# Optimization experiments

Hardware: AMD Instinct MI355X
Metric: run time of the kernel (lower is better)

The kernel has to match this reference:

```python
import jax, jax.numpy as jnp
import numpy as np

D = 2048
N_HEAD = 16
D_HEAD = D // N_HEAD
EXP = 4
EPS = 1e-6


def setup_inputs() -> dict:
    key = jax.random.key(0)
    ks = jax.random.split(key, 8)
    b, s = 2, 2048
    scale = 0.02
    return {
        "x": jax.random.normal(ks[0], (b, s, D), dtype=jnp.float32),
        "w_qkv": jax.random.normal(ks[1], (D, 3 * D), dtype=jnp.float32) * scale,
        "w_o": jax.random.normal(ks[2], (D, D), dtype=jnp.float32) * scale,
        "w_up": jax.random.normal(ks[3], (D, EXP * D), dtype=jnp.float32) * scale,
        "w_gate": jax.random.normal(ks[4], (D, EXP * D), dtype=jnp.float32) * scale,
        "w_down": jax.random.normal(ks[5], (EXP * D, D), dtype=jnp.float32) * scale,
        "scale1": jnp.ones((D,), dtype=jnp.float32),
        "scale2": jnp.ones((D,), dtype=jnp.float32),
    }


def _rmsnorm(x, scale):
    rms = jnp.sqrt(jnp.mean(x * x, axis=-1, keepdims=True) + EPS)
    return x / rms * scale


def _attention(x, w_qkv, w_o):
    b, s, d = x.shape
    qkv = x @ w_qkv  # [b, s, 3d]
    q, k, v = jnp.split(qkv, 3, axis=-1)
    # [b, h, s, dh]
    q = q.reshape(b, s, N_HEAD, D_HEAD).transpose(0, 2, 1, 3)
    k = k.reshape(b, s, N_HEAD, D_HEAD).transpose(0, 2, 1, 3)
    v = v.reshape(b, s, N_HEAD, D_HEAD).transpose(0, 2, 1, 3)
    scores = jnp.einsum("bhqd,bhkd->bhqk", q, k) / np.sqrt(D_HEAD).astype(np.float32)
    causal = jnp.tril(jnp.ones((s, s), dtype=bool))
    scores = jnp.where(causal, scores, -jnp.inf)
    attn = jax.nn.softmax(scores, axis=-1)
    out = jnp.einsum("bhqk,bhkd->bhqd", attn, v)
    out = out.transpose(0, 2, 1, 3).reshape(b, s, d)
    return out @ w_o


def _mlp(x, w_up, w_gate, w_down):
    return (x @ w_up * jax.nn.silu(x @ w_gate)) @ w_down


def reference(x, w_qkv, w_o, w_up, w_gate, w_down, scale1, scale2):
    x = x + _attention(_rmsnorm(x, scale1), w_qkv, w_o)
    x = x + _mlp(_rmsnorm(x, scale2), w_up, w_gate, w_down)
    return x
```

## Files before the change

kernel.cpp:

```cpp
#include <hip/hip_runtime.h>

typedef unsigned short u16;
typedef __bf16 bfrag8 __attribute__((ext_vector_type(8)));
typedef float f32x4 __attribute__((ext_vector_type(4)));

#define MFMA16(a, b, c) __builtin_amdgcn_mfma_f32_16x16x32_bf16((a), (b), (c), 0, 0, 0)

static __device__ __forceinline__ u16 bf_bits(float f) {
  unsigned int u = __builtin_bit_cast(unsigned int, f);
  unsigned int r = (u + 0x7fffu + ((u >> 16) & 1u)) >> 16;
  return (u16)r;
}
static __device__ __forceinline__ float f_from_bits(u16 u) {
  unsigned int w = ((unsigned int)u) << 16;
  return __builtin_bit_cast(float, w);
}
static __device__ __forceinline__ void gload16(const void* g, void* l) {
  __builtin_amdgcn_global_load_lds(
      (const __attribute__((address_space(1))) void*)g,
      (__attribute__((address_space(3))) void*)l, 16, 0, 0);
}

__global__ __launch_bounds__(256) void k_transpose_bf16(const float* __restrict__ src,
                                                        u16* __restrict__ dst,
                                                        int K, int N) {
  __shared__ float tile[32][33];
  const int n0 = blockIdx.x * 32;
  const int k0 = blockIdx.y * 32;
  const int t = threadIdx.x;
  const int lr = t >> 5;
  const int lc = t & 31;
#pragma unroll
  for (int i = 0; i < 4; ++i)
    tile[lr + i * 8][lc] = src[(size_t)(k0 + lr + i * 8) * N + n0 + lc];
  __syncthreads();
#pragma unroll
  for (int i = 0; i < 4; ++i)
    dst[(size_t)(n0 + lr + i * 8) * K + k0 + lc] = bf_bits(tile[lc][lr + i * 8]);
}

__global__ __launch_bounds__(256) void k_transpose_v(const u16* __restrict__ qkv,
                                                     u16* __restrict__ vtg) {
  __shared__ u16 tile[32][33];
  const int bh = blockIdx.z, b = bh >> 4, hh = bh & 15;
  const int s0 = blockIdx.x * 32, d0 = blockIdx.y * 32;
  const int t = threadIdx.x;
  const int lr = t >> 5, lc = t & 31;
#pragma unroll
  for (int i = 0; i < 4; ++i)
    tile[lr + i * 8][lc] =
        qkv[(size_t)(b * 2048 + s0 + lr + i * 8) * 6144 + 4096 + hh * 128 + d0 + lc];
  __syncthreads();
#pragma unroll
  for (int i = 0; i < 4; ++i)
    vtg[(size_t)bh * 128 * 2048 + (size_t)(d0 + lr + i * 8) * 2048 + s0 + lc] =
        tile[lc][lr + i * 8];
}

__global__ __launch_bounds__(256) void k_rmsnorm(const float* __restrict__ x,
                                                 const float* __restrict__ sc,
                                                 u16* __restrict__ o) {
  const int row = blockIdx.x;
  const int t = threadIdx.x;
  const float4* x4 = (const float4*)(x + (size_t)row * 2048);
  float4 a = x4[t];
  float4 b = x4[t + 256];
  float ss = a.x * a.x + a.y * a.y + a.z * a.z + a.w * a.w +
             b.x * b.x + b.y * b.y + b.z * b.z + b.w * b.w;
#pragma unroll
  for (int off = 32; off > 0; off >>= 1) ss += __shfl_down(ss, off);
  __shared__ float red[4];
  if ((t & 63) == 0) red[t >> 6] = ss;
  __syncthreads();
  const float inv = rsqrtf((red[0] + red[1] + red[2] + red[3]) * (1.0f / 2048.0f) + 1e-6f);
  const float4* s4 = (const float4*)sc;
  float4 sa = s4[t], sb = s4[t + 256];
  ushort4 pa, pb;
  pa.x = bf_bits(a.x * inv * sa.x); pa.y = bf_bits(a.y * inv * sa.y);
  pa.z = bf_bits(a.z * inv * sa.z); pa.w = bf_bits(a.w * inv * sa.w);
  pb.x = bf_bits(b.x * inv * sb.x); pb.y = bf_bits(b.y * inv * sb.y);
  pb.z = bf_bits(b.z * inv * sb.z); pb.w = bf_bits(b.w * inv * sb.w);
  *(ushort4*)(o + (size_t)row * 2048 + t * 4) = pa;
  *(ushort4*)(o + (size_t)row * 2048 + (t + 256) * 4) = pb;
}

template <int EPI, int K, int PART>
__global__ __launch_bounds__(256, 3) void k_gemm2(const u16* __restrict__ A,
                                                  const u16* __restrict__ Bt,
                                                  int N,
                                                  float* __restrict__ outF,
                                                  u16* __restrict__ outB,
                                                  const float* __restrict__ resid) {
  __shared__ u16 sm[24576];
  char* smC = (char*)sm;
  const int nbx = gridDim.x;
  const int f = blockIdx.x + nbx * blockIdx.y;
  int m0, np;
  if (PART == 0) {
    const int nsl = nbx >> 3;
    const int x = f & 7;
    const int j = f >> 3;
    np = x * nsl + (j % nsl);
    m0 = (j / nsl) * 128;
  } else {
    const int msl = (int)gridDim.y >> 3;
    const int x = f & 7;
    const int j = f >> 3;
    m0 = (x * msl + (j % msl)) * 128;
    np = j / msl;
  }
  const int n0 = np * 256;

  const int t = threadIdx.x;
  const int wid = t >> 6, lane = t & 63;
  const int wm = wid >> 1, wn = wid & 1;
  const int l15 = lane & 15, lhi = lane >> 4;
  const int lhi16 = lhi * 16;
  const int swz = (l15 & 7) << 4;

  f32x4 acc0[4][4], acc1[4][4];
#pragma unroll
  for (int i = 0; i < 4; ++i)
#pragma unroll
    for (int j2 = 0; j2 < 4; ++j2) {
      acc0[i][j2] = (f32x4){0.f, 0.f, 0.f, 0.f};
      acc1[i][j2] = (f32x4){0.f, 0.f, 0.f, 0.f};
    }

  const int sr = lane >> 3;
  const int csw = (((lane & 7) * 16) ^ (sr << 4)) >> 1;
  const u16* Asrc = A + (size_t)(m0 + wid * 32 + sr) * K + csw;
  const u16* B0src = Bt + (size_t)(n0 + wid * 32 + sr) * K + csw;
  const u16* B1src = Bt + (size_t)(n0 + 128 + wid * 32 + sr) * K + csw;
  char* adst = smC + wid * 4096 + lane * 16;
  char* b0dst = smC + 16384 + wid * 4096 + lane * 16;
  char* b1dst = smC + 32768 + wid * 4096 + lane * 16;

  for (int kt = 0; kt < K / 64; ++kt) {
    __syncthreads();
    const u16* as = Asrc + kt * 64;
    const u16* b0s = B0src + kt * 64;
    const u16* b1s = B1src + kt * 64;
#pragma unroll
    for (int c = 0; c < 4; ++c) {
      gload16(as + (size_t)c * 8 * K, adst + c * 1024);
      gload16(b0s + (size_t)c * 8 * K, b0dst + c * 1024);
      gload16(b1s + (size_t)c * 8 * K, b1dst + c * 1024);
    }
    asm volatile("s_waitcnt vmcnt(0)" ::: "memory");
    __syncthreads();

#pragma unroll
    for (int kh = 0; kh < 2; ++kh) {
      const int ko = (kh * 64 + lhi16);
      bfrag8 a0 = *(const bfrag8*)(smC + (wm * 64 + 0 * 16 + l15) * 128 + (ko ^ swz));
      bfrag8 a1 = *(const bfrag8*)(smC + (wm * 64 + 1 * 16 + l15) * 128 + (ko ^ swz));
      bfrag8 a2 = *(const bfrag8*)(smC + (wm * 64 + 2 * 16 + l15) * 128 + (ko ^ swz));
      bfrag8 a3 = *(const bfrag8*)(smC + (wm * 64 + 3 * 16 + l15) * 128 + (ko ^ swz));
      bfrag8 g0 = *(const bfrag8*)(smC + 16384 + (wn * 64 + 0 * 16 + l15) * 128 + (ko ^ swz));
      bfrag8 g1 = *(const bfrag8*)(smC + 16384 + (wn * 64 + 1 * 16 + l15) * 128 + (ko ^ swz));
      bfrag8 g2 = *(const bfrag8*)(smC + 16384 + (wn * 64 + 2 * 16 + l15) * 128 + (ko ^ swz));
      bfrag8 g3 = *(const bfrag8*)(smC + 16384 + (wn * 64 + 3 * 16 + l15) * 128 + (ko ^ swz));
      acc0[0][0] = MFMA16(a0, g0, acc0[0][0]); acc0[0][1] = MFMA16(a0, g1, acc0[0][1]);
      acc0[0][2] = MFMA16(a0, g2, acc0[0][2]); acc0[0][3] = MFMA16(a0, g3, acc0[0][3]);
      acc0[1][0] = MFMA16(a1, g0, acc0[1][0]); acc0[1][1] = MFMA16(a1, g1, acc0[1][1]);
      acc0[1][2] = MFMA16(a1, g2, acc0[1][2]); acc0[1][3] = MFMA16(a1, g3, acc0[1][3]);
      acc0[2][0] = MFMA16(a2, g0, acc0[2][0]); acc0[2][1] = MFMA16(a2, g1, acc0[2][1]);
      acc0[2][2] = MFMA16(a2, g2, acc0[2][2]); acc0[2][3] = MFMA16(a2, g3, acc0[2][3]);
      acc0[3][0] = MFMA16(a3, g0, acc0[3][0]); acc0[3][1] = MFMA16(a3, g1, acc0[3][1]);
      acc0[3][2] = MFMA16(a3, g2, acc0[3][2]); acc0[3][3] = MFMA16(a3, g3, acc0[3][3]);
      bfrag8 u0 = *(const bfrag8*)(smC + 32768 + (wn * 64 + 0 * 16 + l15) * 128 + (ko ^ swz));
      bfrag8 u1 = *(const bfrag8*)(smC + 32768 + (wn * 64 + 1 * 16 + l15) * 128 + (ko ^ swz));
      bfrag8 u2 = *(const bfrag8*)(smC + 32768 + (wn * 64 + 2 * 16 + l15) * 128 + (ko ^ swz));
      bfrag8 u3 = *(const bfrag8*)(smC + 32768 + (wn * 64 + 3 * 16 + l15) * 128 + (ko ^ swz));
      acc1[0][0] = MFMA16(a0, u0, acc1[0][0]); acc1[0][1] = MFMA16(a0, u1, acc1[0][1]);
      acc1[0][2] = MFMA16(a0, u2, acc1[0][2]); acc1[0][3] = MFMA16(a0, u3, acc1[0][3]);
      acc1[1][0] = MFMA16(a1, u0, acc1[1][0]); acc1[1][1] = MFMA16(a1, u1, acc1[1][1]);
      acc1[1][2] = MFMA16(a1, u2, acc1[1][2]); acc1[1][3] = MFMA16(a1, u3, acc1[1][3]);
      acc1[2][0] = MFMA16(a2, u0, acc1[2][0]); acc1[2][1] = MFMA16(a2, u1, acc1[2][1]);
      acc1[2][2] = MFMA16(a2, u2, acc1[2][2]); acc1[2][3] = MFMA16(a2, u3, acc1[2][3]);
      acc1[3][0] = MFMA16(a3, u0, acc1[3][0]); acc1[3][1] = MFMA16(a3, u1, acc1[3][1]);
      acc1[3][2] = MFMA16(a3, u2, acc1[3][2]); acc1[3][3] = MFMA16(a3, u3, acc1[3][3]);
    }
  }

#pragma unroll
  for (int h = 0; h < 2; ++h) {
#pragma unroll
    for (int i = 0; i < 4; ++i) {
#pragma unroll
      for (int j2 = 0; j2 < 4; ++j2) {
        const int mr = m0 + wm * 64 + i * 16 + lhi * 4;
        const int nc = n0 + h * 128 + wn * 64 + j2 * 16 + l15;
#pragma unroll
        for (int r = 0; r < 4; ++r) {
          const size_t idx = (size_t)(mr + r) * N + nc;
          const float v = h ? acc1[i][j2][r] : acc0[i][j2][r];
          if (EPI == 0) {
            outB[idx] = bf_bits(v);
          } else {
            outF[idx] = resid[idx] + v;
          }
        }
      }
    }
  }
}

template <int K>
__global__ __launch_bounds__(256, 3) void k_gemm_mlp(const u16* __restrict__ A,
                                                     const u16* __restrict__ Bg,
                                                     const u16* __restrict__ Bu,
                                                     int N,
                                                     u16* __restrict__ outB) {
  __shared__ u16 sm[24576];
  char* smC = (char*)sm;
  const int nbx = gridDim.x;
  const int f = blockIdx.x + nbx * blockIdx.y;
  const int nsl = nbx >> 3;
  const int x = f & 7;
  const int j = f >> 3;
  const int n0 = (x * nsl + (j % nsl)) * 128;
  const int m0 = (j / nsl) * 128;

  const int t = threadIdx.x;
  const int wid = t >> 6, lane = t & 63;
  const int wm = wid >> 1, wn = wid & 1;
  const int l15 = lane & 15, lhi = lane >> 4;
  const int lhi16 = lhi * 16;
  const int swz = (l15 & 7) << 4;

  f32x4 accg[4][4], accu[4][4];
#pragma unroll
  for (int i = 0; i < 4; ++i)
#pragma unroll
    for (int j2 = 0; j2 < 4; ++j2) {
      accg[i][j2] = (f32x4){0.f, 0.f, 0.f, 0.f};
      accu[i][j2] = (f32x4){0.f, 0.f, 0.f, 0.f};
    }

  const int sr = lane >> 3;
  const int csw = (((lane & 7) * 16) ^ (sr << 4)) >> 1;
  const u16* Asrc = A + (size_t)(m0 + wid * 32 + sr) * K + csw;
  const u16* Bgsrc = Bg + (size_t)(n0 + wid * 32 + sr) * K + csw;
  const u16* Busrc = Bu + (size_t)(n0 + wid * 32 + sr) * K + csw;
  char* adst = smC + wid * 4096 + lane * 16;
  char* bgdst = smC + 16384 + wid * 4096 + lane * 16;
  char* budst = smC + 32768 + wid * 4096 + lane * 16;

  for (int kt = 0; kt < K / 64; ++kt) {
    __syncthreads();
    const u16* as = Asrc + kt * 64;
    const u16* gs = Bgsrc + kt * 64;
    const u16* us = Busrc + kt * 64;
#pragma unroll
    for (int c = 0; c < 4; ++c) {
      gload16(as + (size_t)c * 8 * K, adst + c * 1024);
      gload16(gs + (size_t)c * 8 * K, bgdst + c * 1024);
      gload16(us + (size_t)c * 8 * K, budst + c * 1024);
    }
    asm volatile("s_waitcnt vmcnt(0)" ::: "memory");
    __syncthreads();

#pragma unroll
    for (int kh = 0; kh < 2; ++kh) {
      const int ko = (kh * 64 + lhi16);
      bfrag8 a0 = *(const bfrag8*)(smC + (wm * 64 + 0 * 16 + l15) * 128 + (ko ^ swz));
      bfrag8 a1 = *(const bfrag8*)(smC + (wm * 64 + 1 * 16 + l15) * 128 + (ko ^ swz));
      bfrag8 a2 = *(const bfrag8*)(smC + (wm * 64 + 2 * 16 + l15) * 128 + (ko ^ swz));
      bfrag8 a3 = *(const bfrag8*)(smC + (wm * 64 + 3 * 16 + l15) * 128 + (ko ^ swz));
      bfrag8 g0 = *(const bfrag8*)(smC + 16384 + (wn * 64 + 0 * 16 + l15) * 128 + (ko ^ swz));
      bfrag8 g1 = *(const bfrag8*)(smC + 16384 + (wn * 64 + 1 * 16 + l15) * 128 + (ko ^ swz));
      bfrag8 g2 = *(const bfrag8*)(smC + 16384 + (wn * 64 + 2 * 16 + l15) * 128 + (ko ^ swz));
      bfrag8 g3 = *(const bfrag8*)(smC + 16384 + (wn * 64 + 3 * 16 + l15) * 128 + (ko ^ swz));
      accg[0][0] = MFMA16(a0, g0, accg[0][0]); accg[0][1] = MFMA16(a0, g1, accg[0][1]);
      accg[0][2] = MFMA16(a0, g2, accg[0][2]); accg[0][3] = MFMA16(a0, g3, accg[0][3]);
      accg[1][0] = MFMA16(a1, g0, accg[1][0]); accg[1][1] = MFMA16(a1, g1, accg[1][1]);
      accg[1][2] = MFMA16(a1, g2, accg[1][2]); accg[1][3] = MFMA16(a1, g3, accg[1][3]);
      accg[2][0] = MFMA16(a2, g0, accg[2][0]); accg[2][1] = MFMA16(a2, g1, accg[2][1]);
      accg[2][2] = MFMA16(a2, g2, accg[2][2]); accg[2][3] = MFMA16(a2, g3, accg[2][3]);
      accg[3][0] = MFMA16(a3, g0, accg[3][0]); accg[3][1] = MFMA16(a3, g1, accg[3][1]);
      accg[3][2] = MFMA16(a3, g2, accg[3][2]); accg[3][3] = MFMA16(a3, g3, accg[3][3]);
      bfrag8 u0 = *(const bfrag8*)(smC + 32768 + (wn * 64 + 0 * 16 + l15) * 128 + (ko ^ swz));
      bfrag8 u1 = *(const bfrag8*)(smC + 32768 + (wn * 64 + 1 * 16 + l15) * 128 + (ko ^ swz));
      bfrag8 u2 = *(const bfrag8*)(smC + 32768 + (wn * 64 + 2 * 16 + l15) * 128 + (ko ^ swz));
      bfrag8 u3 = *(const bfrag8*)(smC + 32768 + (wn * 64 + 3 * 16 + l15) * 128 + (ko ^ swz));
      accu[0][0] = MFMA16(a0, u0, accu[0][0]); accu[0][1] = MFMA16(a0, u1, accu[0][1]);
      accu[0][2] = MFMA16(a0, u2, accu[0][2]); accu[0][3] = MFMA16(a0, u3, accu[0][3]);
      accu[1][0] = MFMA16(a1, u0, accu[1][0]); accu[1][1] = MFMA16(a1, u1, accu[1][1]);
      accu[1][2] = MFMA16(a1, u2, accu[1][2]); accu[1][3] = MFMA16(a1, u3, accu[1][3]);
      accu[2][0] = MFMA16(a2, u0, accu[2][0]); accu[2][1] = MFMA16(a2, u1, accu[2][1]);
      accu[2][2] = MFMA16(a2, u2, accu[2][2]); accu[2][3] = MFMA16(a2, u3, accu[2][3]);
      accu[3][0] = MFMA16(a3, u0, accu[3][0]); accu[3][1] = MFMA16(a3, u1, accu[3][1]);
      accu[3][2] = MFMA16(a3, u2, accu[3][2]); accu[3][3] = MFMA16(a3, u3, accu[3][3]);
    }
  }

#pragma unroll
  for (int i = 0; i < 4; ++i) {
#pragma unroll
    for (int j2 = 0; j2 < 4; ++j2) {
      const int mr = m0 + wm * 64 + i * 16 + lhi * 4;
      const int nc = n0 + wn * 64 + j2 * 16 + l15;
#pragma unroll
      for (int r = 0; r < 4; ++r) {
        const float g = accg[i][j2][r];
        const float u = accu[i][j2][r];
        const float s = g / (1.f + __expf(-g));
        outB[(size_t)(mr + r) * N + nc] = bf_bits(u * s);
      }
    }
  }
}

__global__ __launch_bounds__(512) void k_attn(const u16* __restrict__ qkv,
                                              const u16* __restrict__ vtg,
                                              u16* __restrict__ out) {
  const int S = 2048, LD = 6144;
  const float scale = 0.0883883476483184405f;
  const int fid = blockIdx.x;
  const int p = fid >> 1, s = fid & 1;
  const int bh = p & 31;
  const int pq = p >> 5;
  const int qt = s ? (15 - pq) : pq;
  const int b = bh >> 4, hh = bh & 15;
  const int t = threadIdx.x;
  const int wave = t >> 6, lane = t & 63;
  const int l15 = lane & 15, lhi = lane >> 4;
  const int lhi16 = lhi * 16;
  const int swz = (l15 & 7) << 4;

  __shared__ u16 Kt[64 * 128];
  __shared__ u16 Vt[128 * 64];
  __shared__ u16 Pl[8][16][72];
  char* KtC = (char*)Kt;
  char* VtC = (char*)Vt;

  const int qrow = qt * 128 + wave * 16 + l15;
  const size_t qoff = (size_t)(b * S + qrow) * LD + hh * 128 + lhi * 8;
  bfrag8 qf[4];
#pragma unroll
  for (int ks = 0; ks < 4; ++ks) qf[ks] = *(const bfrag8*)(qkv + qoff + ks * 32);

  f32x4 oacc[8];
#pragma unroll
  for (int j = 0; j < 8; ++j) oacc[j] = (f32x4){0.f, 0.f, 0.f, 0.f};
  float m_i[4], l_i[4];
#pragma unroll
  for (int r = 0; r < 4; ++r) { m_i[r] = -INFINITY; l_i[r] = 0.f; }

  const int q_my = qt * 128 + wave * 16 + lhi * 4;
  const int q_wave_last = qt * 128 + wave * 16 + 15;

  const int keyA = t >> 4, keyB = 32 + (t >> 4);
  const int oK = (t & 15) * 16;
  const int dA = t >> 3, dB = 64 + (t >> 3);
  const int oV = (t & 7) * 16;
  const u16* kbase = qkv + (size_t)(b * S) * LD + 2048 + hh * 128;
  const u16* vbase = vtg + (size_t)bh * 128 * S;
  const u16* ksrcA = kbase + (size_t)keyA * LD + ((oK ^ ((keyA & 7) << 4)) >> 1);
  const u16* ksrcB = kbase + (size_t)keyB * LD + ((oK ^ ((keyB & 7) << 4)) >> 1);
  const u16* vsrcA = vbase + (size_t)dA * S + ((oV ^ ((dA & 7) << 4)) >> 1);
  const u16* vsrcB = vbase + (size_t)dB * S + ((oV ^ ((dB & 7) << 4)) >> 1);
  const unsigned int ldso0 = wave * 1024 + lane * 16;
  const unsigned int ldso1 = 8192 + wave * 1024 + lane * 16;
  const size_t kstep = (size_t)64 * LD;

  const int kt_max = 2 * qt + 1;
  for (int kt = 0; kt <= kt_max; ++kt) {
    __syncthreads();
    gload16(ksrcA + (size_t)kt * kstep, KtC + ldso0);
    gload16(ksrcB + (size_t)kt * kstep, KtC + ldso1);
    gload16(vsrcA + kt * 64, VtC + ldso0);
    gload16(vsrcB + kt * 64, VtC + ldso1);
    __syncthreads();

    if (kt * 64 <= q_wave_last) {
      f32x4 sfr[4];
#pragma unroll
      for (int j = 0; j < 4; ++j) {
        sfr[j] = (f32x4){0.f, 0.f, 0.f, 0.f};
        const int krow = j * 16 + l15;
#pragma unroll
        for (int ks = 0; ks < 4; ++ks) {
          bfrag8 kf = *(const bfrag8*)(KtC + krow * 256 + ((ks * 64 + lhi16) ^ swz));
          sfr[j] = MFMA16(qf[ks], kf, sfr[j]);
        }
      }
      float sv[4][4], rmax[4];
#pragma unroll
      for (int r = 0; r < 4; ++r) rmax[r] = -INFINITY;
#pragma unroll
      for (int j = 0; j < 4; ++j) {
        const int key = kt * 64 + j * 16 + l15;
#pragma unroll
        for (int r = 0; r < 4; ++r) {
          float v = sfr[j][r] * scale;
          v = (key <= q_my + r) ? v : -INFINITY;
          sv[j][r] = v;
          rmax[r] = fmaxf(rmax[r], v);
        }
      }
#pragma unroll
      for (int r = 0; r < 4; ++r) {
        float v = rmax[r];
        v = fmaxf(v, __shfl_xor(v, 1));
        v = fmaxf(v, __shfl_xor(v, 2));
        v = fmaxf(v, __shfl_xor(v, 4));
        v = fmaxf(v, __shfl_xor(v, 8));
        rmax[r] = v;
      }
      float alpha[4], rsum[4];
#pragma unroll
      for (int r = 0; r < 4; ++r) {
        float mn = fmaxf(m_i[r], rmax[r]);
        alpha[r] = __expf(m_i[r] - mn);
        m_i[r] = mn;
        rsum[r] = 0.f;
      }
#pragma unroll
      for (int j = 0; j < 4; ++j) {
#pragma unroll
        for (int r = 0; r < 4; ++r) {
          float p2 = __expf(sv[j][r] - m_i[r]);
          rsum[r] += p2;
          Pl[wave][lhi * 4 + r][j * 16 + l15] = bf_bits(p2);
        }
      }
#pragma unroll
      for (int r = 0; r < 4; ++r) {
        float v = rsum[r];
        v += __shfl_xor(v, 1); v += __shfl_xor(v, 2);
        v += __shfl_xor(v, 4); v += __shfl_xor(v, 8);
        l_i[r] = l_i[r] * alpha[r] + v;
      }
#pragma unroll
      for (int j = 0; j < 8; ++j)
#pragma unroll
        for (int r = 0; r < 4; ++r) oacc[j][r] *= alpha[r];

#pragma unroll
      for (int ks2 = 0; ks2 < 2; ++ks2) {
        bfrag8 pf = *(const bfrag8*)&Pl[wave][l15][ks2 * 32 + lhi * 8];
#pragma unroll
        for (int j = 0; j < 8; ++j) {
          const int d = j * 16 + l15;
          bfrag8 vf = *(const bfrag8*)(VtC + d * 128 + ((ks2 * 64 + lhi16) ^ swz));
          oacc[j] = MFMA16(pf, vf, oacc[j]);
        }
      }
    }
  }

#pragma unroll
  for (int r = 0; r < 4; ++r) {
    const float inv = 1.f / l_i[r];
    const size_t tok = (size_t)b * S + qt * 128 + wave * 16 + lhi * 4 + r;
#pragma unroll
    for (int j = 0; j < 8; ++j)
      out[tok * 2048 + hh * 128 + j * 16 + l15] = bf_bits(oacc[j][r] * inv);
  }
}

extern "C" void kernel_launch(void* const* d_in, const int* in_sizes, int n_in,
                              void* d_out, int out_size, void* d_ws, size_t ws_size,
                              hipStream_t stream) {
  (void)in_sizes; (void)n_in; (void)out_size; (void)ws_size;
  const float* x      = (const float*)d_in[0];
  const float* w_qkv  = (const float*)d_in[1];
  const float* w_o    = (const float*)d_in[2];
  const float* w_up   = (const float*)d_in[3];
  const float* w_gate = (const float*)d_in[4];
  const float* w_down = (const float*)d_in[5];
  const float* scale1 = (const float*)d_in[6];
  const float* scale2 = (const float*)d_in[7];
  float* out = (float*)d_out;

  u16* B       = (u16*)d_ws;
  u16* wqkvT   = B;
  u16* woT     = wqkvT  + (size_t)6144 * 2048;
  u16* wgateT  = woT    + (size_t)2048 * 2048;
  u16* wupT    = wgateT + (size_t)8192 * 2048;
  u16* wdownT  = wupT   + (size_t)8192 * 2048;
  u16* xn      = wdownT + (size_t)2048 * 8192;
  u16* qkvb    = xn     + (size_t)4096 * 2048;
  u16* attnb   = qkvb   + (size_t)4096 * 6144;
  float* y1    = (float*)(attnb + (size_t)4096 * 2048);
  u16* vtg     = (u16*)y1;
  u16* hbuf    = qkvb;

  dim3 blk(256);
  k_transpose_bf16<<<dim3(192, 64), blk, 0, stream>>>(w_qkv,  wqkvT,  2048, 6144);
  k_transpose_bf16<<<dim3(64, 64),  blk, 0, stream>>>(w_o,    woT,    2048, 2048);
  k_transpose_bf16<<<dim3(256, 64), blk, 0, stream>>>(w_gate, wgateT, 2048, 8192);
  k_transpose_bf16<<<dim3(256, 64), blk, 0, stream>>>(w_up,   wupT,   2048, 8192);
  k_transpose_bf16<<<dim3(64, 256), blk, 0, stream>>>(w_down, wdownT, 8192, 2048);

  k_rmsnorm<<<4096, blk, 0, stream>>>(x, scale1, xn);
  k_gemm2<0, 2048, 0><<<dim3(24, 32), blk, 0, stream>>>(xn, wqkvT, 6144, nullptr, qkvb, nullptr);
  k_transpose_v<<<dim3(64, 4, 32), blk, 0, stream>>>(qkvb, vtg);
  k_attn<<<dim3(512), dim3(512), 0, stream>>>(qkvb, vtg, attnb);
  k_gemm2<1, 2048, 1><<<dim3(8, 32), blk, 0, stream>>>(attnb, woT, 2048, y1, nullptr, x);
  k_rmsnorm<<<4096, blk, 0, stream>>>(y1, scale2, xn);
  k_gemm_mlp<2048><<<dim3(64, 32), blk, 0, stream>>>(xn, wgateT, wupT, 8192, hbuf);
  k_gemm2<1, 8192, 1><<<dim3(8, 32), blk, 0, stream>>>(hbuf, wdownT, 2048, out, nullptr, y1);
}
```

Baseline: 947.6 us.

## Use 128x128-tile GEMM kernel for output and down projections

Adds a new k_gemm kernel with 128x128 tiles, a 64-wide K step, swizzled LDS loads via global_load_lds, and 4 blocks per CU. The O-projection and down-projection, both with N=2048, move from k_gemm2 on an 8x32 grid to this kernel on a 16x32 grid. The aim is to launch more blocks so more of the CUs are busy on these narrow GEMMs. In exchange there is less data reuse per tile and only one LDS buffer, with a full vmcnt(0) wait and barrier every K step, so loads are not overlapped with the MFMAs.

After: 817.8 us (median of 2 runs). -13.7%, faster.

```diff
diff --git a/kernel.cpp b/kernel.cpp
--- a/kernel.cpp
+++ b/kernel.cpp
@@ -82,6 +82,111 @@
   pb.z = bf_bits(b.z * inv * sb.z); pb.w = bf_bits(b.w * inv * sb.w);
   *(ushort4*)(o + (size_t)row * 2048 + t * 4) = pa;
   *(ushort4*)(o + (size_t)row * 2048 + (t + 256) * 4) = pb;
+}
+
+template <int EPI, int K, int PART>
+__global__ __launch_bounds__(256, 4) void k_gemm(const u16* __restrict__ A,
+                                                 const u16* __restrict__ Bt,
+                                                 int M, int N,
+                                                 float* __restrict__ outF,
+                                                 u16* __restrict__ outB,
+                                                 const float* __restrict__ resid,
+                                                 const u16* __restrict__ gate) {
+  __shared__ u16 sm[16384];
+  char* smC = (char*)sm;
+  const int nbx = gridDim.x;
+  const int f = blockIdx.x + nbx * blockIdx.y;
+  int m0, n0;
+  if (PART == 0) {
+    const int nsl = nbx >> 3;
+    const int x = f & 7;
+    const int j = f >> 3;
+    n0 = (x * nsl + (j % nsl)) * 128;
+    m0 = (j / nsl) * 128;
+  } else {
+    const int msl = (int)gridDim.y >> 3;
+    const int x = f & 7;
+    const int j = f >> 3;
+    m0 = (x * msl + (j % msl)) * 128;
+    n0 = (j / msl) * 128;
+  }
+
+  const int t = threadIdx.x;
+  const int wid = t >> 6, lane = t & 63;
+  const int wm = wid >> 1, wn = wid & 1;
+  const int l15 = lane & 15, lhi = lane >> 4;
+  const int lhi16 = lhi * 16;
+  const int swz = (l15 & 7) << 4;
+
+  f32x4 acc[4][4];
+#pragma unroll
+  for (int i = 0; i < 4; ++i)
+#pragma unroll
+    for (int j2 = 0; j2 < 4; ++j2) acc[i][j2] = (f32x4){0.f, 0.f, 0.f, 0.f};
+
+  const int sr = lane >> 3;
+  const int csw = (((lane & 7) * 16) ^ (sr << 4)) >> 1;
+  const u16* Asrc = A + (size_t)(m0 + wid * 32 + sr) * K + csw;
+  const u16* Bsrc = Bt + (size_t)(n0 + wid * 32 + sr) * K + csw;
+  char* adst = smC + wid * 4096 + lane * 16;
+  char* bdst = smC + 16384 + wid * 4096 + lane * 16;
+
+  for (int kt = 0; kt < K / 64; ++kt) {
+    __syncthreads();
+    const u16* as = Asrc + kt * 64;
+    const u16* bs = Bsrc + kt * 64;
+#pragma unroll
+    for (int c = 0; c < 4; ++c) {
+      gload16(as + (size_t)c * 8 * K, adst + c * 1024);
+      gload16(bs + (size_t)c * 8 * K, bdst + c * 1024);
+    }
+    asm volatile("s_waitcnt vmcnt(0)" ::: "memory");
+    __syncthreads();
+
+#pragma unroll
+    for (int kh = 0; kh < 2; ++kh) {
+      const int ko = kh * 64 + lhi16;
+      bfrag8 a0 = *(const bfrag8*)(smC + (wm * 64 + 0 * 16 + l15) * 128 + (ko ^ swz));
+      bfrag8 a1 = *(const bfrag8*)(smC + (wm * 64 + 1 * 16 + l15) * 128 + (ko ^ swz));
+      bfrag8 a2 = *(const bfrag8*)(smC + (wm * 64 + 2 * 16 + l15) * 128 + (ko ^ swz));
+      bfrag8 a3 = *(const bfrag8*)(smC + (wm * 64 + 3 * 16 + l15) * 128 + (ko ^ swz));
+      bfrag8 b0 = *(const bfrag8*)(smC + 16384 + (wn * 64 + 0 * 16 + l15) * 128 + (ko ^ swz));
+      bfrag8 b1 = *(const bfrag8*)(smC + 16384 + (wn * 64 + 1 * 16 + l15) * 128 + (ko ^ swz));
+      bfrag8 b2 = *(const bfrag8*)(smC + 16384 + (wn * 64 + 2 * 16 + l15) * 128 + (ko ^ swz));
+      bfrag8 b3 = *(const bfrag8*)(smC + 16384 + (wn * 64 + 3 * 16 + l15) * 128 + (ko ^ swz));
+      acc[0][0] = MFMA16(a0, b0, acc[0][0]); acc[0][1] = MFMA16(a0, b1, acc[0][1]);
+      acc[0][2] = MFMA16(a0, b2, acc[0][2]); acc[0][3] = MFMA16(a0, b3, acc[0][3]);
+      acc[1][0] = MFMA16(a1, b0, acc[1][0]); acc[1][1] = MFMA16(a1, b1, acc[1][1]);
+      acc[1][2] = MFMA16(a1, b2, acc[1][2]); acc[1][3] = MFMA16(a1, b3, acc[1][3]);
+      acc[2][0] = MFMA16(a2, b0, acc[2][0]); acc[2][1] = MFMA16(a2, b1, acc[2][1]);
+      acc[2][2] = MFMA16(a2, b2, acc[2][2]); acc[2][3] = MFMA16(a2, b3, acc[2][3]);
+      acc[3][0] = MFMA16(a3, b0, acc[3][0]); acc[3][1] = MFMA16(a3, b1, acc[3][1]);
+      acc[3][2] = MFMA16(a3, b2, acc[3][2]); acc[3][3] = MFMA16(a3, b3, acc[3][3]);
+    }
+  }
+
+#pragma unroll
+  for (int i = 0; i < 4; ++i) {
+#pragma unroll
+    for (int j2 = 0; j2 < 4; ++j2) {
+      const int mr = m0 + wm * 64 + i * 16 + lhi * 4;
+      const int nc = n0 + wn * 64 + j2 * 16 + l15;
+#pragma unroll
+      for (int r = 0; r < 4; ++r) {
+        const size_t idx = (size_t)(mr + r) * N + nc;
+        const float v = acc[i][j2][r];
+        if (EPI == 0) {
+          outB[idx] = bf_bits(v);
+        } else if (EPI == 1) {
+          outF[idx] = resid[idx] + v;
+        } else {
+          float g = f_from_bits(gate[idx]);
+          float s = g / (1.f + __expf(-g));
+          outB[idx] = bf_bits(v * s);
+        }
+      }
+    }
+  }
 }
 
 template <int EPI, int K, int PART>
@@ -500,8 +605,8 @@
   k_gemm2<0, 2048, 0><<<dim3(24, 32), blk, 0, stream>>>(xn, wqkvT, 6144, nullptr, qkvb, nullptr);
   k_transpose_v<<<dim3(64, 4, 32), blk, 0, stream>>>(qkvb, vtg);
   k_attn<<<dim3(512), dim3(512), 0, stream>>>(qkvb, vtg, attnb);
-  k_gemm2<1, 2048, 1><<<dim3(8, 32), blk, 0, stream>>>(attnb, woT, 2048, y1, nullptr, x);
+  k_gemm<1, 2048, 1><<<dim3(16, 32), blk, 0, stream>>>(attnb, woT, 4096, 2048, y1, nullptr, x, nullptr);
   k_rmsnorm<<<4096, blk, 0, stream>>>(y1, scale2, xn);
   k_gemm_mlp<2048><<<dim3(64, 32), blk, 0, stream>>>(xn, wgateT, wupT, 8192, hbuf);
-  k_gemm2<1, 8192, 1><<<dim3(8, 32), blk, 0, stream>>>(hbuf, wdownT, 2048, out, nullptr, y1);
-}
+  k_gemm<1, 8192, 1><<<dim3(16, 32), blk, 0, stream>>>(hbuf, wdownT, 4096, 2048, out, nullptr, y1, nullptr);
+}
```
